# Kernel optimization log

Measured on AMD Instinct MI355X. Metric: run time of the kernel, lower is better.

## Reference

```python
import jax, jax.numpy as jnp
import numpy as np

EMBED_DIM = 1024
NUM_HEADS = 16
HEAD_DIM = EMBED_DIM // NUM_HEADS
MASKED = True


def setup_inputs() -> dict:
    key = jax.random.key(0)
    ks = jax.random.split(key, 9)
    B, S, E = 4, 2048, EMBED_DIM
    sc = 1.0 / np.sqrt(E)
    return {
        "x": jax.random.normal(ks[0], (B, S, E), jnp.float32),
        "wq": jax.random.normal(ks[1], (E, E), jnp.float32) * sc,
        "bq": jax.random.normal(ks[2], (E,), jnp.float32) * 0.02,
        "wk": jax.random.normal(ks[3], (E, E), jnp.float32) * sc,
        "bk": jax.random.normal(ks[4], (E,), jnp.float32) * 0.02,
        "wv": jax.random.normal(ks[5], (E, E), jnp.float32) * sc,
        "bv": jax.random.normal(ks[6], (E,), jnp.float32) * 0.02,
        "wo": jax.random.normal(ks[7], (E, E), jnp.float32) * sc,
        "bo": jax.random.normal(ks[8], (E,), jnp.float32) * 0.02,
    }


def reference(x, wq, bq, wk, bk, wv, bv, wo, bo):
    B, S, E = x.shape
    H, Dh = NUM_HEADS, HEAD_DIM
    # QKV projections, then split heads: [B,S,E] -> [B,H,S,Dh]
    def split(t):
        return t.reshape(B, S, H, Dh).transpose(0, 2, 1, 3)
    q = split(x @ wq.T + bq)
    k = split(x @ wk.T + bk)
    v = split(x @ wv.T + bv)
    scale = Dh ** 0.5
    scores = jnp.einsum('bhsd,bhtd->bhst', q, k) / scale  # [B,H,S,S]
    if MASKED:
        causal = jnp.tril(jnp.ones((S, S), dtype=bool))
        scores = jnp.where(causal, scores, -jnp.inf)
    weights = jax.nn.softmax(scores, axis=-1)
    ctx = jnp.einsum('bhst,bhtd->bhsd', weights, v)
    ctx = ctx.transpose(0, 2, 1, 3).reshape(B, S, E)
    return ctx @ wo.T + bo
```

## Files before the change

### kernel.cpp

```cpp
#include <hip/hip_runtime.h>
#include <hip/hip_bf16.h>

#define EMB   1024
#define SEQ   2048
#define BATCH 4
#define NH    16
#define DHEAD 64
#define MROWS (BATCH*SEQ)
#define NSTRIP (SEQ/32)
#define QSCALE 0.18033688011112042f

typedef float f32x4  __attribute__((ext_vector_type(4)));
typedef float f32x16 __attribute__((ext_vector_type(16)));
typedef short s16x8  __attribute__((ext_vector_type(8)));

__device__ __forceinline__ f32x4 mfma16(s16x8 a, s16x8 b, f32x4 c) {
    return __builtin_amdgcn_mfma_f32_16x16x32_bf16(a, b, c, 0, 0, 0);
}
__device__ __forceinline__ f32x16 mfma32(s16x8 a, s16x8 b, f32x16 c) {
    return __builtin_amdgcn_mfma_f32_32x32x16_bf16(a, b, c, 0, 0, 0);
}

__device__ __forceinline__ unsigned short f2bf(float f) {
    __hip_bfloat16 h = __float2bfloat16(f);
    return __builtin_bit_cast(unsigned short, h);
}

__device__ __forceinline__ unsigned cvtpk(float lo, float hi) {
    unsigned r;
    asm("v_cvt_pk_bf16_f32 %0, %1, %2" : "=v"(r) : "v"(lo), "v"(hi));
    return r;
}

__device__ __forceinline__ void plane_swap(unsigned &a, unsigned &b) {
    asm("v_permlane32_swap_b32 %0, %1" : "+v"(a), "+v"(b));
}

__device__ __forceinline__ s16x8 frag4(unsigned a, unsigned b, unsigned c, unsigned d) {
    union { unsigned u[4]; s16x8 f; } x;
    x.u[0] = a; x.u[1] = b; x.u[2] = c; x.u[3] = d;
    return x.f;
}

__device__ __forceinline__ float exp2r(float x) {
    float r;
    asm("v_exp_f32 %0, %1" : "=v"(r) : "v"(x));
    return r;
}
__device__ __forceinline__ float max3f(float a, float b, float c) {
    float r;
    asm("v_max3_f32 %0, %1, %2, %3" : "=v"(r) : "v"(a), "v"(b), "v"(c));
    return r;
}

__global__ void cvt_bf16(const float* __restrict__ in, unsigned short* __restrict__ out, int n4) {
    int i = blockIdx.x * blockDim.x + threadIdx.x;
    if (i >= n4) return;
    float4 v = reinterpret_cast<const float4*>(in)[i];
    ushort4 o;
    o.x = f2bf(v.x); o.y = f2bf(v.y); o.z = f2bf(v.z); o.w = f2bf(v.w);
    reinterpret_cast<ushort4*>(out)[i] = o;
}

__global__ void cvt_bf16_w(const float* __restrict__ w0, const float* __restrict__ w1,
                           const float* __restrict__ w2, const float* __restrict__ w3,
                           unsigned short* __restrict__ o0, unsigned short* __restrict__ o1,
                           unsigned short* __restrict__ o2, unsigned short* __restrict__ o3,
                           int n4) {
    int i = blockIdx.x * blockDim.x + threadIdx.x;
    if (i >= n4) return;
    const float* in; unsigned short* out;
    switch (blockIdx.y) {
        case 0:  in = w0; out = o0; break;
        case 1:  in = w1; out = o1; break;
        case 2:  in = w2; out = o2; break;
        default: in = w3; out = o3; break;
    }
    float4 v = reinterpret_cast<const float4*>(in)[i];
    ushort4 o;
    o.x = f2bf(v.x); o.y = f2bf(v.y); o.z = f2bf(v.z); o.w = f2bf(v.w);
    reinterpret_cast<ushort4*>(out)[i] = o;
}

#define GLDS(g, s) __builtin_amdgcn_global_load_lds((const __attribute__((address_space(1))) void*)(g), \
                       (__attribute__((address_space(3))) void*)(s), 16, 0, 0)

__global__ __launch_bounds__(256) void gemm_qkv(const unsigned short* __restrict__ A,
                                                const unsigned short* __restrict__ wqb,
                                                const unsigned short* __restrict__ wkb,
                                                const unsigned short* __restrict__ wvb,
                                                const float* __restrict__ bq,
                                                const float* __restrict__ bk,
                                                const float* __restrict__ bv,
                                                unsigned short* __restrict__ qB,
                                                unsigned short* __restrict__ kB,
                                                unsigned short* __restrict__ vtB) {
    __shared__ unsigned short sA[128*32];
    __shared__ unsigned short sB[128*32];
    const int tid = threadIdx.x;
    const int w  = tid >> 6, l = tid & 63;
    const int lg = l >> 4,  lr = l & 15;
    const int nb  = blockIdx.x;
    const int seg = nb >> 3;
    const int mBase = blockIdx.y * 128;
    const int nBase = (nb & 7) * 128;
    const unsigned short* Bw = (seg == 0) ? wqb : (seg == 1) ? wkb : wvb;
    const float* bias = (seg == 0) ? bq : (seg == 1) ? bk : bv;
    const int wr = w >> 1, wc = w & 1;
    const int srow = l >> 2;
    const int sk0  = (l & 3) * 8;
    const bool segV = (seg == 2);

    f32x4 acc[4][4] = {};

    for (int kb = 0; kb < EMB; kb += 32) {
        __syncthreads();
        #pragma unroll
        for (int rr = 0; rr < 2; ++rr) {
            const int chunk = w + rr * 4;
            const unsigned short* ga = A  + (size_t)(mBase + chunk*16 + srow) * EMB + kb + sk0;
            GLDS(ga, &sA[chunk * 512]);
            const unsigned short* gb = Bw + (size_t)(nBase + chunk*16 + srow) * EMB + kb + sk0;
            GLDS(gb, &sB[chunk * 512]);
        }
        __syncthreads();
        s16x8 af[4], bf[4];
        #pragma unroll
        for (int mi = 0; mi < 4; ++mi)
            af[mi] = *reinterpret_cast<const s16x8*>(&sA[(wr*64 + mi*16 + lr)*32 + lg*8]);
        #pragma unroll
        for (int ni = 0; ni < 4; ++ni)
            bf[ni] = *reinterpret_cast<const s16x8*>(&sB[(wc*64 + ni*16 + lr)*32 + lg*8]);
        if (segV) {
            #pragma unroll
            for (int mi = 0; mi < 4; ++mi)
                #pragma unroll
                for (int ni = 0; ni < 4; ++ni)
                    acc[ni][mi] = mfma16(bf[ni], af[mi], acc[ni][mi]);
        } else {
            #pragma unroll
            for (int mi = 0; mi < 4; ++mi)
                #pragma unroll
                for (int ni = 0; ni < 4; ++ni)
                    acc[mi][ni] = mfma16(af[mi], bf[ni], acc[mi][ni]);
        }
    }

    const int colBase = nBase + wc * 64;
    const int rowBase = mBase + wr * 64;
    if (!segV) {
        unsigned short* outp = seg ? kB : qB;
        const float oscale = seg ? 1.0f : QSCALE;
        #pragma unroll
        for (int ni = 0; ni < 4; ++ni) {
            const int col = colBase + ni*16 + lr;
            const float bv = bias[col];
            const int h = col >> 6, d = col & 63;
            const int inner = ((d >> 4) * 2 + ((d >> 3) & 1)) * 256 + (d & 7);
            #pragma unroll
            for (int mi = 0; mi < 4; ++mi) {
                #pragma unroll
                for (int r = 0; r < 4; ++r) {
                    const int gr = rowBase + mi*16 + lg*4 + r;
                    const int b = gr >> 11, sin_ = gr & 2047;
                    const int strip = sin_ >> 5, l31q = sin_ & 31;
                    outp[(size_t)(b*NH + h) * (SEQ*DHEAD) + strip*2048 + inner + l31q*8]
                        = f2bf((acc[mi][ni][r] + bv) * oscale);
                }
            }
        }
    } else {
        unsigned short* outp = vtB;
        #pragma unroll
        for (int ni = 0; ni < 4; ++ni) {
            #pragma unroll
            for (int r = 0; r < 4; ++r) {
                const int n = colBase + ni*16 + lg*4 + r;
                const float bv = bias[n];
                const int h = n >> 6, d = n & 63;
                #pragma unroll
                for (int mi = 0; mi < 4; ++mi) {
                    const int tok = rowBase + mi*16 + lr;
                    const int b = tok >> 11, sv = tok & 2047;
                    const int kvt = sv >> 5, ks = (sv >> 4) & 1, hi2 = (sv >> 3) & 1, j = sv & 7;
                    outp[(size_t)(b*NH + h) * (SEQ*DHEAD) + kvt*2048 + (ks*2 + hi2)*512 + d*8 + j]
                        = f2bf(acc[ni][mi][r] + bv);
                }
            }
        }
    }
}

__global__ __launch_bounds__(256) void gemm_out(const unsigned short* __restrict__ A,
                                                const unsigned short* __restrict__ Bw,
                                                const float* __restrict__ bias,
                                                float* __restrict__ Out) {
    __shared__ unsigned short sA[128*32];
    __shared__ unsigned short sB[128*32];
    const int tid = threadIdx.x;
    const int w  = tid >> 6, l = tid & 63;
    const int lg = l >> 4,  lr = l & 15;
    const int mBase = blockIdx.y * 128;
    const int nBase = blockIdx.x * 128;
    const int wr = w >> 1, wc = w & 1;
    const int srow = l >> 2;
    const int sk0  = (l & 3) * 8;

    f32x4 acc[4][4] = {};

    for (int kb = 0; kb < EMB; kb += 32) {
        __syncthreads();
        #pragma unroll
        for (int rr = 0; rr < 2; ++rr) {
            const int chunk = w + rr * 4;
            const unsigned short* ga = A  + (size_t)(mBase + chunk*16 + srow) * EMB + kb + sk0;
            GLDS(ga, &sA[chunk * 512]);
            const unsigned short* gb = Bw + (size_t)(nBase + chunk*16 + srow) * EMB + kb + sk0;
            GLDS(gb, &sB[chunk * 512]);
        }
        __syncthreads();
        s16x8 af[4], bf[4];
        #pragma unroll
        for (int mi = 0; mi < 4; ++mi)
            af[mi] = *reinterpret_cast<const s16x8*>(&sA[(wr*64 + mi*16 + lr)*32 + lg*8]);
        #pragma unroll
        for (int ni = 0; ni < 4; ++ni)
            bf[ni] = *reinterpret_cast<const s16x8*>(&sB[(wc*64 + ni*16 + lr)*32 + lg*8]);
        #pragma unroll
        for (int mi = 0; mi < 4; ++mi)
            #pragma unroll
            for (int ni = 0; ni < 4; ++ni)
                acc[mi][ni] = mfma16(af[mi], bf[ni], acc[mi][ni]);
    }

    const int colBase = nBase + wc * 64;
    const int rowBase = mBase + wr * 64;
    #pragma unroll
    for (int ni = 0; ni < 4; ++ni) {
        const int col = colBase + ni*16 + lr;
        const float bv = bias[col];
        #pragma unroll
        for (int mi = 0; mi < 4; ++mi) {
            #pragma unroll
            for (int r = 0; r < 4; ++r) {
                const int gr = rowBase + mi*16 + lg*4 + r;
                Out[(size_t)gr * EMB + col] = acc[mi][ni][r] + bv;
            }
        }
    }
}

__global__ __launch_bounds__(64) void attn_fwd(const unsigned short* __restrict__ qb,
                                               const unsigned short* __restrict__ kb,
                                               const unsigned short* __restrict__ vb,
                                               unsigned short* __restrict__ ctx) {
    __shared__ __align__(16) unsigned sld[32*36];
    const int l = threadIdx.x;
    const int l31 = l & 31, hi = l >> 5;
    const int bh = blockIdx.x & 63;
    const int strip = (NSTRIP - 1) - ((int)blockIdx.x >> 6);
    const int q0 = strip * 32;
    const size_t hbase = (size_t)bh * SEQ * DHEAD;
    const unsigned short* qh = qb + hbase;
    const unsigned short* kh = kb + hbase;
    const unsigned short* vh = vb + hbase;

    s16x8 qf[4];
    #pragma unroll
    for (int s = 0; s < 4; ++s)
        qf[s] = *reinterpret_cast<const s16x8*>(&qh[strip*2048 + s*512 + l*8]);

    f32x16 o0 = {}, o1 = {};
    float m = -__builtin_inff(), lsum = 0.f;
    const int ntiles = strip + 1;

    s16x8 kfA[4], vfA[4], kfB[4], vfB[4];

    auto LOADKV = [&](s16x8* kf, s16x8* vf, int t) {
        const unsigned short* kp = kh + t*2048;
        #pragma unroll
        for (int s = 0; s < 4; ++s)
            kf[s] = *reinterpret_cast<const s16x8*>(&kp[s*512 + l*8]);
        const unsigned short* vp = vh + t*2048 + hi*512 + l31*8;
        #pragma unroll
        for (int ks = 0; ks < 2; ++ks) {
            vf[ks]     = *reinterpret_cast<const s16x8*>(&vp[ks*1024]);
            vf[2 + ks] = *reinterpret_cast<const s16x8*>(&vp[ks*1024 + 256]);
        }
    };

    auto BODY = [&](s16x8* kf, s16x8* vf, int t) {
        f32x16 sa = {};
        #pragma unroll
        for (int s = 0; s < 4; ++s) sa = mfma32(kf[s], qf[s], sa);

        if (t == strip) {
            #pragma unroll
            for (int r = 0; r < 16; ++r) {
                const int kvloc = (r & 3) + 8*(r >> 2) + 4*hi;
                if (kvloc > l31) sa[r] = -__builtin_inff();
            }
        }

        const float a0 = max3f(sa[0],  sa[1],  sa[2]);
        const float a1 = max3f(sa[3],  sa[4],  sa[5]);
        const float a2 = max3f(sa[6],  sa[7],  sa[8]);
        const float a3 = max3f(sa[9],  sa[10], sa[11]);
        const float a4 = max3f(sa[12], sa[13], sa[14]);
        const float b0 = max3f(a0, a1, a2);
        const float b1 = max3f(a3, a4, sa[15]);
        float pm = fmaxf(b0, b1);
        pm = fmaxf(pm, __shfl_xor(pm, 32));

        float mn = m;
        if (!__all(pm <= m + 8.0f)) {
            mn = fmaxf(m, pm);
            const float fs = exp2r(m - mn);
            o0 *= fs; o1 *= fs; lsum *= fs;
            m = mn;
        }

        #pragma unroll
        for (int r = 0; r < 16; ++r) sa[r] = exp2r(sa[r] - mn);

        const float s0 = sa[0]+sa[1],   s1 = sa[2]+sa[3],   s2 = sa[4]+sa[5],   s3 = sa[6]+sa[7];
        const float s4 = sa[8]+sa[9],   s5 = sa[10]+sa[11], s6 = sa[12]+sa[13], s7 = sa[14]+sa[15];
        const float t0 = s0+s1, t1 = s2+s3, t2 = s4+s5, t3 = s6+s7;
        float rs = (t0+t1) + (t2+t3);
        rs += __shfl_xor(rs, 32);
        lsum += rs;

        unsigned u[4], v[4];
        #pragma unroll
        for (int r2 = 0; r2 < 4; ++r2) {
            u[r2] = cvtpk(sa[4*r2 + 0], sa[4*r2 + 1]);
            v[r2] = cvtpk(sa[4*r2 + 2], sa[4*r2 + 3]);
        }
        plane_swap(u[0], u[1]); plane_swap(v[0], v[1]);
        plane_swap(u[2], u[3]); plane_swap(v[2], v[3]);
        const s16x8 pf0 = frag4(u[0], v[0], u[1], v[1]);
        const s16x8 pf1 = frag4(u[2], v[2], u[3], v[3]);

        o0 = mfma32(vf[0], pf0, o0);
        o0 = mfma32(vf[1], pf1, o0);
        o1 = mfma32(vf[2], pf0, o1);
        o1 = mfma32(vf[3], pf1, o1);
    };

    LOADKV(kfA, vfA, 0);
    int t = 0;
    for (; t + 1 < ntiles; t += 2) {
        LOADKV(kfB, vfB, t + 1);
        BODY(kfA, vfA, t);
        if (t + 2 < ntiles) LOADKV(kfA, vfA, t + 2);
        BODY(kfB, vfB, t + 1);
    }
    if (t < ntiles) BODY(kfA, vfA, t);

    const float inv = 1.0f / lsum;
    #pragma unroll
    for (int dt = 0; dt < 2; ++dt) {
        #pragma unroll
        for (int r2 = 0; r2 < 4; ++r2) {
            const float e0 = (dt ? o1[4*r2+0] : o0[4*r2+0]) * inv;
            const float e1 = (dt ? o1[4*r2+1] : o0[4*r2+1]) * inv;
            const float e2 = (dt ? o1[4*r2+2] : o0[4*r2+2]) * inv;
            const float e3 = (dt ? o1[4*r2+3] : o0[4*r2+3]) * inv;
            const int col = 4*r2 + 2*hi + 16*dt;
            sld[l31*36 + col]     = cvtpk(e0, e1);
            sld[l31*36 + col + 1] = cvtpk(e2, e3);
        }
    }
    asm volatile("s_waitcnt lgkmcnt(0)" ::: "memory");
    __builtin_amdgcn_sched_barrier(0);
    const int row = l >> 1, half = l & 1;
    const unsigned* rp = &sld[row*36 + half*16];
    const int b = bh >> 4, h = bh & 15;
    unsigned short* op = &ctx[((size_t)b*SEQ + q0 + row) * EMB + h*DHEAD + half*32];
    #pragma unroll
    for (int i = 0; i < 4; ++i) {
        uint4 d4 = *reinterpret_cast<const uint4*>(rp + i*4);
        *reinterpret_cast<uint4*>(op + i*8) = d4;
    }
}

extern "C" void kernel_launch(void* const* d_in, const int* in_sizes, int n_in,
                              void* d_out, int out_size, void* d_ws, size_t ws_size,
                              hipStream_t stream) {
    const float* x  = (const float*)d_in[0];
    const float* wq = (const float*)d_in[1];
    const float* bq = (const float*)d_in[2];
    const float* wk = (const float*)d_in[3];
    const float* bk = (const float*)d_in[4];
    const float* wv = (const float*)d_in[5];
    const float* bv = (const float*)d_in[6];
    const float* wo = (const float*)d_in[7];
    const float* bo = (const float*)d_in[8];
    float* out = (float*)d_out;

    char* ws = (char*)d_ws;
    const size_t MB = 1ull << 20;
    unsigned short* xb  = (unsigned short*)(ws);
    unsigned short* wqb = (unsigned short*)(ws + 16*MB);
    unsigned short* wkb = (unsigned short*)(ws + 18*MB);
    unsigned short* wvb = (unsigned short*)(ws + 20*MB);
    unsigned short* wob = (unsigned short*)(ws + 22*MB);
    unsigned short* qB  = (unsigned short*)(ws + 24*MB);
    unsigned short* kB  = (unsigned short*)(ws + 40*MB);
    unsigned short* vtB = (unsigned short*)(ws + 56*MB);
    unsigned short* ctx = xb;

    const int nx4 = MROWS * EMB / 4;
    const int nw4 = EMB * EMB / 4;
    cvt_bf16<<<(nx4 + 255)/256, 256, 0, stream>>>(x, xb, nx4);
    cvt_bf16_w<<<dim3((nw4 + 255)/256, 4), 256, 0, stream>>>(wq, wk, wv, wo, wqb, wkb, wvb, wob, nw4);

    gemm_qkv<<<dim3(24, MROWS/128), 256, 0, stream>>>(xb, wqb, wkb, wvb, bq, bk, bv, qB, kB, vtB);

    attn_fwd<<<dim3(NSTRIP * BATCH * NH), 64, 0, stream>>>(qB, kB, vtB, ctx);

    gemm_out<<<dim3(EMB/128, MROWS/128), 256, 0, stream>>>(ctx, wob, bo, out);
}
```

Before: 184.9 us.

## Double-buffer LDS tiles in QKV and output projection GEMMs

Both projection GEMMs now use two LDS buffers per operand. The next K-slice is issued via global_load_lds into one buffer while MFMAs consume the other, and the barrier count per K step is halved. The goal is to hide global-load latency behind compute. It doubles LDS use per block, which may reduce occupancy. Correctness relies on __syncthreads ordering the direct-to-LDS loads before they are read.

Measured after the change: 183.8 us. Within noise of the previous version (-0.6%).

```diff
diff --git a/kernel.cpp b/kernel.cpp
--- a/kernel.cpp
+++ b/kernel.cpp
@@ -95,8 +95,10 @@
                                                 unsigned short* __restrict__ qB,
                                                 unsigned short* __restrict__ kB,
                                                 unsigned short* __restrict__ vtB) {
-    __shared__ unsigned short sA[128*32];
-    __shared__ unsigned short sB[128*32];
+    __shared__ unsigned short sA0[128*32];
+    __shared__ unsigned short sB0[128*32];
+    __shared__ unsigned short sA1[128*32];
+    __shared__ unsigned short sB1[128*32];
     const int tid = threadIdx.x;
     const int w  = tid >> 6, l = tid & 63;
     const int lg = l >> 4,  lr = l & 15;
@@ -113,24 +115,24 @@
 
     f32x4 acc[4][4] = {};
 
-    for (int kb = 0; kb < EMB; kb += 32) {
-        __syncthreads();
+    auto STAGE = [&](unsigned short* dA, unsigned short* dB, int kb) {
         #pragma unroll
         for (int rr = 0; rr < 2; ++rr) {
             const int chunk = w + rr * 4;
             const unsigned short* ga = A  + (size_t)(mBase + chunk*16 + srow) * EMB + kb + sk0;
-            GLDS(ga, &sA[chunk * 512]);
+            GLDS(ga, &dA[chunk * 512]);
             const unsigned short* gb = Bw + (size_t)(nBase + chunk*16 + srow) * EMB + kb + sk0;
-            GLDS(gb, &sB[chunk * 512]);
-        }
-        __syncthreads();
+            GLDS(gb, &dB[chunk * 512]);
+        }
+    };
+    auto COMPUTE = [&](const unsigned short* dA, const unsigned short* dB) {
         s16x8 af[4], bf[4];
         #pragma unroll
         for (int mi = 0; mi < 4; ++mi)
-            af[mi] = *reinterpret_cast<const s16x8*>(&sA[(wr*64 + mi*16 + lr)*32 + lg*8]);
+            af[mi] = *reinterpret_cast<const s16x8*>(&dA[(wr*64 + mi*16 + lr)*32 + lg*8]);
         #pragma unroll
         for (int ni = 0; ni < 4; ++ni)
-            bf[ni] = *reinterpret_cast<const s16x8*>(&sB[(wc*64 + ni*16 + lr)*32 + lg*8]);
+            bf[ni] = *reinterpret_cast<const s16x8*>(&dB[(wc*64 + ni*16 + lr)*32 + lg*8]);
         if (segV) {
             #pragma unroll
             for (int mi = 0; mi < 4; ++mi)
@@ -144,6 +146,17 @@
                 for (int ni = 0; ni < 4; ++ni)
                     acc[mi][ni] = mfma16(af[mi], bf[ni], acc[mi][ni]);
         }
+    };
+
+    STAGE(sA0, sB0, 0);
+    __syncthreads();
+    for (int kb = 0; kb < EMB; kb += 64) {
+        STAGE(sA1, sB1, kb + 32);
+        COMPUTE(sA0, sB0);
+        __syncthreads();
+        if (kb + 64 < EMB) STAGE(sA0, sB0, kb + 64);
+        COMPUTE(sA1, sB1);
+        __syncthreads();
     }
 
     const int colBase = nBase + wc * 64;
@@ -195,8 +208,10 @@
                                                 const unsigned short* __restrict__ Bw,
                                                 const float* __restrict__ bias,
                                                 float* __restrict__ Out) {
-    __shared__ unsigned short sA[128*32];
-    __shared__ unsigned short sB[128*32];
+    __shared__ unsigned short sA0[128*32];
+    __shared__ unsigned short sB0[128*32];
+    __shared__ unsigned short sA1[128*32];
+    __shared__ unsigned short sB1[128*32];
     const int tid = threadIdx.x;
     const int w  = tid >> 6, l = tid & 63;
     const int lg = l >> 4,  lr = l & 15;
@@ -208,29 +223,40 @@
 
     f32x4 acc[4][4] = {};
 
-    for (int kb = 0; kb < EMB; kb += 32) {
-        __syncthreads();
+    auto STAGE = [&](unsigned short* dA, unsigned short* dB, int kb) {
         #pragma unroll
         for (int rr = 0; rr < 2; ++rr) {
             const int chunk = w + rr * 4;
             const unsigned short* ga = A  + (size_t)(mBase + chunk*16 + srow) * EMB + kb + sk0;
-            GLDS(ga, &sA[chunk * 512]);
+            GLDS(ga, &dA[chunk * 512]);
             const unsigned short* gb = Bw + (size_t)(nBase + chunk*16 + srow) * EMB + kb + sk0;
-            GLDS(gb, &sB[chunk * 512]);
-        }
-        __syncthreads();
+            GLDS(gb, &dB[chunk * 512]);
+        }
+    };
+    auto COMPUTE = [&](const unsigned short* dA, const unsigned short* dB) {
         s16x8 af[4], bf[4];
         #pragma unroll
         for (int mi = 0; mi < 4; ++mi)
-            af[mi] = *reinterpret_cast<const s16x8*>(&sA[(wr*64 + mi*16 + lr)*32 + lg*8]);
+            af[mi] = *reinterpret_cast<const s16x8*>(&dA[(wr*64 + mi*16 + lr)*32 + lg*8]);
         #pragma unroll
         for (int ni = 0; ni < 4; ++ni)
-            bf[ni] = *reinterpret_cast<const s16x8*>(&sB[(wc*64 + ni*16 + lr)*32 + lg*8]);
+            bf[ni] = *reinterpret_cast<const s16x8*>(&dB[(wc*64 + ni*16 + lr)*32 + lg*8]);
         #pragma unroll
         for (int mi = 0; mi < 4; ++mi)
             #pragma unroll
             for (int ni = 0; ni < 4; ++ni)
                 acc[mi][ni] = mfma16(af[mi], bf[ni], acc[mi][ni]);
+    };
+
+    STAGE(sA0, sB0, 0);
+    __syncthreads();
+    for (int kb = 0; kb < EMB; kb += 64) {
+        STAGE(sA1, sB1, kb + 32);
+        COMPUTE(sA0, sB0);
+        __syncthreads();
+        if (kb + 64 < EMB) STAGE(sA0, sB0, kb + 64);
+        COMPUTE(sA1, sB1);
+        __syncthreads();
     }
 
     const int colBase = nBase + wc * 64;
```

## Replace QKV and output GEMMs with double-buffered 8-wave 256x128 pipelined kernel

Applied to the files above, without the earlier changes.

Both projection GEMMs now share a core that uses 512 threads, a 256x128 output tile and a K step of 64 held in double-buffered LDS (96 KB). Global-to-LDS loads for the next tile are interleaved with MFMA groups, using explicit barriers, vmcnt waits, setprio and a swizzled LDS layout to avoid bank conflicts. The aim is to hide memory latency and cut the per-iteration syncthreads stalls of the old single-buffered 128x128 kernel. The large LDS footprint limits occupancy to about one block per CU, and the hand-placed wait counts are fragile.

After: 194.7 us. 5.3% more time.

```diff
diff --git a/kernel.cpp b/kernel.cpp
--- a/kernel.cpp
+++ b/kernel.cpp
@@ -85,70 +85,132 @@
 #define GLDS(g, s) __builtin_amdgcn_global_load_lds((const __attribute__((address_space(1))) void*)(g), \
                        (__attribute__((address_space(3))) void*)(s), 16, 0, 0)
 
-__global__ __launch_bounds__(256) void gemm_qkv(const unsigned short* __restrict__ A,
-                                                const unsigned short* __restrict__ wqb,
-                                                const unsigned short* __restrict__ wkb,
-                                                const unsigned short* __restrict__ wvb,
-                                                const float* __restrict__ bq,
-                                                const float* __restrict__ bk,
-                                                const float* __restrict__ bv,
-                                                unsigned short* __restrict__ qB,
-                                                unsigned short* __restrict__ kB,
-                                                unsigned short* __restrict__ vtB) {
-    __shared__ unsigned short sA[128*32];
-    __shared__ unsigned short sB[128*32];
+#define MEMF asm volatile("" ::: "memory")
+#define SBAR __builtin_amdgcn_s_barrier()
+
+#define STA_(buf, kb, s) GLDS(Ag + (kb) + (s)*16, (buf) + (s)*8192 + wbase)
+#define STB_(buf, kb, u) GLDS(Bg + (kb) + (u)*32, (buf) + (u)*8192 + wbase)
+#define LDA_(buf, ks, mi) (*(const s16x8*)((buf) + (ks)*16384 + (lg>>1)*8192 + \
+        (wm*64 + (mi)*16 + lr)*32 + (((lg&1) ^ rdsw))*16))
+#define LDB_(buf, ks, ni) (*(const s16x8*)((buf) + (ks)*8192 + (lg>>1)*4096 + \
+        (wn*64 + (ni)*16 + lr)*32 + (((lg&1) ^ rdsw))*16))
+
+#define MMGRP(MH) \
+    if constexpr (SWAP) { \
+        acc[0][MH]     = mfma16(q0, af0, acc[0][MH]); \
+        acc[1][MH]     = mfma16(q1, af0, acc[1][MH]); \
+        acc[2][MH]     = mfma16(q2, af0, acc[2][MH]); \
+        acc[3][MH]     = mfma16(q3, af0, acc[3][MH]); \
+        acc[0][(MH)+1] = mfma16(q0, af1, acc[0][(MH)+1]); \
+        acc[1][(MH)+1] = mfma16(q1, af1, acc[1][(MH)+1]); \
+        acc[2][(MH)+1] = mfma16(q2, af1, acc[2][(MH)+1]); \
+        acc[3][(MH)+1] = mfma16(q3, af1, acc[3][(MH)+1]); \
+    } else { \
+        acc[MH][0]     = mfma16(af0, q0, acc[MH][0]); \
+        acc[MH][1]     = mfma16(af0, q1, acc[MH][1]); \
+        acc[MH][2]     = mfma16(af0, q2, acc[MH][2]); \
+        acc[MH][3]     = mfma16(af0, q3, acc[MH][3]); \
+        acc[(MH)+1][0] = mfma16(af1, q0, acc[(MH)+1][0]); \
+        acc[(MH)+1][1] = mfma16(af1, q1, acc[(MH)+1][1]); \
+        acc[(MH)+1][2] = mfma16(af1, q2, acc[(MH)+1][2]); \
+        acc[(MH)+1][3] = mfma16(af1, q3, acc[(MH)+1][3]); \
+    }
+
+#define TILE_(CA, CB, NA, NB, KBN, STG) { \
+     \
+    s16x8 q0 = LDB_(CB,0,0), q1 = LDB_(CB,0,1), q2 = LDB_(CB,0,2), q3 = LDB_(CB,0,3); \
+    s16x8 af0 = LDA_(CA,0,0), af1 = LDA_(CA,0,1); \
+    if (STG) { STA_(NA, KBN, 0); } \
+    MEMF; SBAR; \
+    __builtin_amdgcn_s_setprio(1); MMGRP(0); __builtin_amdgcn_s_setprio(0); \
+    MEMF; SBAR; MEMF; \
+     \
+    af0 = LDA_(CA,0,2); af1 = LDA_(CA,0,3); \
+    if (STG) { STA_(NA, KBN, 1); STB_(NB, KBN, 0); } \
+    MEMF; SBAR; \
+    __builtin_amdgcn_s_setprio(1); MMGRP(2); __builtin_amdgcn_s_setprio(0); \
+    if (STG) { asm volatile("s_waitcnt vmcnt(3)" ::: "memory"); } \
+    else     { asm volatile("s_waitcnt vmcnt(0)" ::: "memory"); } \
+    MEMF; SBAR; MEMF; \
+     \
+    q0 = LDB_(CB,1,0); q1 = LDB_(CB,1,1); q2 = LDB_(CB,1,2); q3 = LDB_(CB,1,3); \
+    af0 = LDA_(CA,1,0); af1 = LDA_(CA,1,1); \
+    if (STG) { STA_(NA, KBN, 2); } \
+    MEMF; SBAR; \
+    __builtin_amdgcn_s_setprio(1); MMGRP(0); __builtin_amdgcn_s_setprio(0); \
+    MEMF; SBAR; MEMF; \
+     \
+    af0 = LDA_(CA,1,2); af1 = LDA_(CA,1,3); \
+    if (STG) { STA_(NA, KBN, 3); STB_(NB, KBN, 1); } \
+    MEMF; SBAR; \
+    __builtin_amdgcn_s_setprio(1); MMGRP(2); __builtin_amdgcn_s_setprio(0); \
+    if (STG) { asm volatile("s_waitcnt vmcnt(3)" ::: "memory"); } \
+    MEMF; SBAR; MEMF; \
+}
+
+template<bool SWAP>
+__device__ __forceinline__ void gemm8p_core(const unsigned short* __restrict__ A,
+                                            const unsigned short* __restrict__ Bw,
+                                            int mBase, int nBase,
+                                            f32x4 (&acc)[4][4], char* lds)
+{
     const int tid = threadIdx.x;
-    const int w  = tid >> 6, l = tid & 63;
-    const int lg = l >> 4,  lr = l & 15;
+    const int w = tid >> 6, l = tid & 63;
+    const int lg = l >> 4, lr = l & 15;
+    const int wm = w & 3, wn = w >> 2;
+    char* const A0 = lds;
+    char* const A1 = lds + 32768;
+    char* const B0 = lds + 65536;
+    char* const B1 = lds + 81920;
+    const int wbase = w * 1024;
+    const int rdsw = (lr >> 2) & 1;
+    const int swz  = (tid >> 3) & 1;
+    const int skh  = (tid & 1) ^ swz;
+    const unsigned short* Ag = A  + (size_t)(mBase + (tid >> 1)) * EMB + skh * 8;
+    const unsigned short* Bg = Bw + (size_t)(nBase + ((tid >> 1) & 127)) * EMB
+                                  + (tid >> 8) * 16 + skh * 8;
+
+    STA_(A0, 0, 0); STA_(A0, 0, 1); STB_(B0, 0, 0);
+    STA_(A0, 0, 2); STA_(A0, 0, 3); STB_(B0, 0, 1);
+    asm volatile("s_waitcnt vmcnt(3)" ::: "memory");
+    SBAR; MEMF;
+
+    for (int t = 0; t < 16; t += 2) {
+        TILE_(A0, B0, A1, B1, (t+1)*64, true);
+        TILE_(A1, B1, A0, B0, (t+2)*64, (t+2) < 16);
+    }
+}
+
+__global__ __launch_bounds__(512) void gemm_qkv8(const unsigned short* __restrict__ A,
+                                                 const unsigned short* __restrict__ wqb,
+                                                 const unsigned short* __restrict__ wkb,
+                                                 const unsigned short* __restrict__ wvb,
+                                                 const float* __restrict__ bq,
+                                                 const float* __restrict__ bk,
+                                                 const float* __restrict__ bv,
+                                                 unsigned short* __restrict__ qB,
+                                                 unsigned short* __restrict__ kB,
+                                                 unsigned short* __restrict__ vtB) {
+    __shared__ __align__(16) char lds[98304];
     const int nb  = blockIdx.x;
     const int seg = nb >> 3;
-    const int mBase = blockIdx.y * 128;
+    const int mBase = blockIdx.y * 256;
     const int nBase = (nb & 7) * 128;
     const unsigned short* Bw = (seg == 0) ? wqb : (seg == 1) ? wkb : wvb;
     const float* bias = (seg == 0) ? bq : (seg == 1) ? bk : bv;
-    const int wr = w >> 1, wc = w & 1;
-    const int srow = l >> 2;
-    const int sk0  = (l & 3) * 8;
-    const bool segV = (seg == 2);
+
+    const int tid = threadIdx.x;
+    const int w = tid >> 6, l = tid & 63;
+    const int lg = l >> 4, lr = l & 15;
+    const int wm = w & 3, wn = w >> 2;
 
     f32x4 acc[4][4] = {};
-
-    for (int kb = 0; kb < EMB; kb += 32) {
-        __syncthreads();
-        #pragma unroll
-        for (int rr = 0; rr < 2; ++rr) {
-            const int chunk = w + rr * 4;
-            const unsigned short* ga = A  + (size_t)(mBase + chunk*16 + srow) * EMB + kb + sk0;
-            GLDS(ga, &sA[chunk * 512]);
-            const unsigned short* gb = Bw + (size_t)(nBase + chunk*16 + srow) * EMB + kb + sk0;
-            GLDS(gb, &sB[chunk * 512]);
-        }
-        __syncthreads();
-        s16x8 af[4], bf[4];
-        #pragma unroll
-        for (int mi = 0; mi < 4; ++mi)
-            af[mi] = *reinterpret_cast<const s16x8*>(&sA[(wr*64 + mi*16 + lr)*32 + lg*8]);
-        #pragma unroll
-        for (int ni = 0; ni < 4; ++ni)
-            bf[ni] = *reinterpret_cast<const s16x8*>(&sB[(wc*64 + ni*16 + lr)*32 + lg*8]);
-        if (segV) {
-            #pragma unroll
-            for (int mi = 0; mi < 4; ++mi)
-                #pragma unroll
-                for (int ni = 0; ni < 4; ++ni)
-                    acc[ni][mi] = mfma16(bf[ni], af[mi], acc[ni][mi]);
-        } else {
-            #pragma unroll
-            for (int mi = 0; mi < 4; ++mi)
-                #pragma unroll
-                for (int ni = 0; ni < 4; ++ni)
-                    acc[mi][ni] = mfma16(af[mi], bf[ni], acc[mi][ni]);
-        }
-    }
-
-    const int colBase = nBase + wc * 64;
-    const int rowBase = mBase + wr * 64;
-    if (!segV) {
+    if (seg == 2) gemm8p_core<true >(A, Bw, mBase, nBase, acc, lds);
+    else          gemm8p_core<false>(A, Bw, mBase, nBase, acc, lds);
+
+    const int colBase = nBase + wn * 64;
+    const int rowBase = mBase + wm * 64;
+    if (seg != 2) {
         unsigned short* outp = seg ? kB : qB;
         const float oscale = seg ? 1.0f : QSCALE;
         #pragma unroll
@@ -170,7 +232,6 @@
             }
         }
     } else {
-        unsigned short* outp = vtB;
         #pragma unroll
         for (int ni = 0; ni < 4; ++ni) {
             #pragma unroll
@@ -183,7 +244,7 @@
                     const int tok = rowBase + mi*16 + lr;
                     const int b = tok >> 11, sv = tok & 2047;
                     const int kvt = sv >> 5, ks = (sv >> 4) & 1, hi2 = (sv >> 3) & 1, j = sv & 7;
-                    outp[(size_t)(b*NH + h) * (SEQ*DHEAD) + kvt*2048 + (ks*2 + hi2)*512 + d*8 + j]
+                    vtB[(size_t)(b*NH + h) * (SEQ*DHEAD) + kvt*2048 + (ks*2 + hi2)*512 + d*8 + j]
                         = f2bf(acc[ni][mi][r] + bv);
                 }
             }
@@ -191,50 +252,23 @@
     }
 }
 
-__global__ __launch_bounds__(256) void gemm_out(const unsigned short* __restrict__ A,
-                                                const unsigned short* __restrict__ Bw,
-                                                const float* __restrict__ bias,
-                                                float* __restrict__ Out) {
-    __shared__ unsigned short sA[128*32];
-    __shared__ unsigned short sB[128*32];
+__global__ __launch_bounds__(512) void gemm_out8(const unsigned short* __restrict__ A,
+                                                 const unsigned short* __restrict__ Bw,
+                                                 const float* __restrict__ bias,
+                                                 float* __restrict__ Out) {
+    __shared__ __align__(16) char lds[98304];
+    const int mBase = blockIdx.y * 256;
+    const int nBase = blockIdx.x * 128;
     const int tid = threadIdx.x;
-    const int w  = tid >> 6, l = tid & 63;
-    const int lg = l >> 4,  lr = l & 15;
-    const int mBase = blockIdx.y * 128;
-    const int nBase = blockIdx.x * 128;
-    const int wr = w >> 1, wc = w & 1;
-    const int srow = l >> 2;
-    const int sk0  = (l & 3) * 8;
+    const int w = tid >> 6, l = tid & 63;
+    const int lg = l >> 4, lr = l & 15;
+    const int wm = w & 3, wn = w >> 2;
 
     f32x4 acc[4][4] = {};
-
-    for (int kb = 0; kb < EMB; kb += 32) {
-        __syncthreads();
-        #pragma unroll
-        for (int rr = 0; rr < 2; ++rr) {
-            const int chunk = w + rr * 4;
-            const unsigned short* ga = A  + (size_t)(mBase + chunk*16 + srow) * EMB + kb + sk0;
-            GLDS(ga, &sA[chunk * 512]);
-            const unsigned short* gb = Bw + (size_t)(nBase + chunk*16 + srow) * EMB + kb + sk0;
-            GLDS(gb, &sB[chunk * 512]);
-        }
-        __syncthreads();
-        s16x8 af[4], bf[4];
-        #pragma unroll
-        for (int mi = 0; mi < 4; ++mi)
-            af[mi] = *reinterpret_cast<const s16x8*>(&sA[(wr*64 + mi*16 + lr)*32 + lg*8]);
-        #pragma unroll
-        for (int ni = 0; ni < 4; ++ni)
-            bf[ni] = *reinterpret_cast<const s16x8*>(&sB[(wc*64 + ni*16 + lr)*32 + lg*8]);
-        #pragma unroll
-        for (int mi = 0; mi < 4; ++mi)
-            #pragma unroll
-            for (int ni = 0; ni < 4; ++ni)
-                acc[mi][ni] = mfma16(af[mi], bf[ni], acc[mi][ni]);
-    }
-
-    const int colBase = nBase + wc * 64;
-    const int rowBase = mBase + wr * 64;
+    gemm8p_core<false>(A, Bw, mBase, nBase, acc, lds);
+
+    const int colBase = nBase + wn * 64;
+    const int rowBase = mBase + wm * 64;
     #pragma unroll
     for (int ni = 0; ni < 4; ++ni) {
         const int col = colBase + ni*16 + lr;
@@ -415,9 +449,9 @@
     cvt_bf16<<<(nx4 + 255)/256, 256, 0, stream>>>(x, xb, nx4);
     cvt_bf16_w<<<dim3((nw4 + 255)/256, 4), 256, 0, stream>>>(wq, wk, wv, wo, wqb, wkb, wvb, wob, nw4);
 
-    gemm_qkv<<<dim3(24, MROWS/128), 256, 0, stream>>>(xb, wqb, wkb, wvb, bq, bk, bv, qB, kB, vtB);
+    gemm_qkv8<<<dim3(24, MROWS/256), 512, 0, stream>>>(xb, wqb, wkb, wvb, bq, bk, bv, qB, kB, vtB);
 
     attn_fwd<<<dim3(NSTRIP * BATCH * NH), 64, 0, stream>>>(qB, kB, vtB, ctx);
 
-    gemm_out<<<dim3(EMB/128, MROWS/128), 256, 0, stream>>>(ctx, wob, bo, out);
-}
+    gemm_out8<<<dim3(EMB/128, MROWS/256), 512, 0, stream>>>(ctx, wob, bo, out);
+}
```
